# Kernel optimization log

Hardware: AMD Instinct MI355X
Metric: run time of the kernel (lower is better)

Reference implementation:

```python
import jax, jax.numpy as jnp
import numpy as np

EPS = 1e-5  # config.layer_norm_epsilon

def setup_inputs() -> dict:
    key = jax.random.key(0)
    ks = jax.random.split(key, 8)
    B, S, D, BOT, N = 8, 2048, 1024, 400, 25
    x = jax.random.normal(ks[0], (B, S, D), dtype=jnp.float32)
    alphas = jax.random.uniform(ks[1], (N,), dtype=jnp.float32) / N
    W_down_all = jax.random.normal(ks[2], (N, BOT, D), dtype=jnp.float32) * 0.02
    W_up_all = jax.random.normal(ks[3], (N, D, BOT), dtype=jnp.float32) * 0.02
    b_down_all = jax.random.normal(ks[4], (N, BOT), dtype=jnp.float32) * 0.02
    b_up_all = jax.random.normal(ks[5], (N, D), dtype=jnp.float32) * 0.02
    W_ln_all = 1.0 + jax.random.normal(ks[6], (N, D), dtype=jnp.float32) * 0.02
    b_ln_all = jax.random.normal(ks[7], (N, D), dtype=jnp.float32) * 0.02
    return {"x": x, "alphas": alphas, "W_down_all": W_down_all, "W_up_all": W_up_all,
            "b_down_all": b_down_all, "b_up_all": b_up_all,
            "W_ln_all": W_ln_all, "b_ln_all": b_ln_all}

def reference(x, alphas, W_down_all, W_up_all, b_down_all, b_up_all, W_ln_all, b_ln_all):
    # Superposition: alpha-weighted sum of all adapters' parameters
    # (original python loop over 25 adapters -> single einsum per tensor).
    W_down = jnp.einsum('n,nbd->bd', alphas, W_down_all)  # [BOT, D]
    W_up   = jnp.einsum('n,ndb->db', alphas, W_up_all)    # [D, BOT]
    W_ln   = jnp.einsum('n,nd->d',  alphas, W_ln_all)     # [D]
    b_ln   = jnp.einsum('n,nd->d',  alphas, b_ln_all)     # [D]
    # b_up / b_down are merged in the original too but passed with bias=None: unused.

    # FAdapter: F.layer_norm with normalized_shape = x.shape[1:], i.e. normalize
    # jointly over (seq, embd) per batch element; ln weight/bias broadcast over seq.
    mu = jnp.mean(x, axis=(1, 2), keepdims=True)
    var = jnp.mean(jnp.square(x - mu), axis=(1, 2), keepdims=True)
    x_ = (x - mu) * jax.lax.rsqrt(var + EPS) * W_ln + b_ln  # [B,S,D]

    h = jax.nn.relu(jnp.einsum('bsd,od->bso', x_, W_down))  # [B,S,BOT], no bias
    x_ = jnp.einsum('bso,do->bsd', h, W_up)                 # [B,S,D],   no bias
    return x + x_
```

## Files before the change

### kernel.cpp

```cpp
#include <hip/hip_runtime.h>
#include <stdint.h>

#define NB   8
#define SS   2048
#define DD   1024
#define BOT  400
#define BOTP 512
#define NAD  25
#define LN_EPS 1e-5f
#define NCH  128

typedef __attribute__((ext_vector_type(8))) short bf8_t;
typedef __attribute__((ext_vector_type(4))) float fx4;

__device__ __forceinline__ unsigned short f2bf(float f) {
  unsigned int u = __float_as_uint(f);
  u = (u + 0x7FFFu + ((u >> 16) & 1u)) >> 16;
  return (unsigned short)u;
}
__device__ __forceinline__ uint32_t cvtpk(float lo, float hi) {
  uint32_t r;
  asm("v_cvt_pk_bf16_f32 %0, %1, %2" : "=v"(r) : "v"(lo), "v"(hi));
  return r;
}

__device__ __forceinline__ void gload16(void* lds, const void* g) {
  __builtin_amdgcn_global_load_lds(
      (const __attribute__((address_space(1))) void*)(uintptr_t)g,
      (__attribute__((address_space(3))) void*)(uint32_t)(uintptr_t)lds,
      16, 0, 0);
}

__global__ __launch_bounds__(256) void mixstats_kernel(
    const float* __restrict__ alphas,
    const float* __restrict__ WdAll, const float* __restrict__ WuAll,
    const float* __restrict__ wlnAll, const float* __restrict__ blnAll,
    const float* __restrict__ x,
    unsigned short* __restrict__ Wd, unsigned short* __restrict__ Wu,
    float* __restrict__ wln, float* __restrict__ bln,
    float* __restrict__ partials)
{
  const int tid = threadIdx.x;
  const int bid = blockIdx.x;

  if (bid >= 920) {
    const int g = bid - 920;
    const int b = g >> 7, c = g & 127;
    const float4* xb = (const float4*)(x + (size_t)b * SS * DD) + (size_t)c * 4096;
    float4 v[16];
#pragma unroll
    for (int i = 0; i < 16; ++i) v[i] = xb[i * 256 + tid];
    __builtin_amdgcn_sched_barrier(0);
    float s = 0.f, q = 0.f;
#pragma unroll
    for (int i = 0; i < 16; ++i) {
      s += v[i].x + v[i].y + v[i].z + v[i].w;
      q += v[i].x * v[i].x + v[i].y * v[i].y + v[i].z * v[i].z + v[i].w * v[i].w;
    }
#pragma unroll
    for (int off = 32; off > 0; off >>= 1) { s += __shfl_down(s, off); q += __shfl_down(q, off); }
    __shared__ float red[8];
    const int wave = tid >> 6, lane = tid & 63;
    if (!lane) { red[wave] = s; red[wave + 4] = q; }
    __syncthreads();
    if (!tid) {
      partials[(b * NCH + c) * 2]     = red[0] + red[1] + red[2] + red[3];
      partials[(b * NCH + c) * 2 + 1] = red[4] + red[5] + red[6] + red[7];
    }
    return;
  }

  __shared__ float a[NAD];
  if (tid < NAD) a[tid] = alphas[tid];
  __syncthreads();

  if (bid < 800) {
    const int g = (bid < 400 ? bid : bid - 400) * 256 + tid;
    const float4* src = (const float4*)(bid < 400 ? WdAll : WuAll) + g;
    float4 vals[NAD];
#pragma unroll
    for (int n = 0; n < NAD; ++n) vals[n] = src[(size_t)n * 102400];
    __builtin_amdgcn_sched_barrier(0);
    float4 acc = {0.f, 0.f, 0.f, 0.f};
#pragma unroll
    for (int n = 0; n < NAD; ++n) {
      acc.x += a[n] * vals[n].x; acc.y += a[n] * vals[n].y;
      acc.z += a[n] * vals[n].z; acc.w += a[n] * vals[n].w;
    }
    uint2 pk = { cvtpk(acc.x, acc.y), cvtpk(acc.z, acc.w) };
    if (bid < 400) {
      *(uint2*)(Wd + (size_t)g * 4) = pk;
    } else {
      const int d = g / 100, bg = g - d * 100;
      *(uint2*)(Wu + (size_t)d * BOTP + bg * 4) = pk;
    }
  } else if (bid < 808) {
    const int i = (bid - 800) * 256 + tid;
    const float* src = (i < DD) ? wlnAll : blnAll;
    const int j = (i < DD) ? i : (i - DD);
    float v[NAD];
#pragma unroll
    for (int n = 0; n < NAD; ++n) v[n] = src[(size_t)n * DD + j];
    __builtin_amdgcn_sched_barrier(0);
    float s = 0.f;
#pragma unroll
    for (int n = 0; n < NAD; ++n) s += a[n] * v[n];
    if (i < DD) wln[j] = s; else bln[j] = s;
  } else if (bid < 864) {
    const int t = (bid - 808) * 256 + tid;
    int4 z = {0, 0, 0, 0};
    *(int4*)(Wd + 400 * 1024 + (size_t)t * 8) = z;
  } else {
    const int t = (bid - 864) * 256 + tid;
    const int row = t / 14, c8 = t - row * 14;
    int4 z = {0, 0, 0, 0};
    *(int4*)(Wu + (size_t)row * BOTP + 400 + c8 * 8) = z;
  }
}

__global__ __launch_bounds__(256) void norm_kernel(const float* __restrict__ x,
    const float* __restrict__ partials, const float* __restrict__ wln,
    const float* __restrict__ bln, unsigned short* __restrict__ xn)
{
  const int b = blockIdx.y;
  double sd = 0.0, qd = 0.0;
#pragma unroll 8
  for (int i = 0; i < NCH; ++i) {
    sd += partials[(b * NCH + i) * 2];
    qd += partials[(b * NCH + i) * 2 + 1];
  }
  const float mu  = (float)(sd * (1.0 / 2097152.0));
  const float var = (float)(qd * (1.0 / 2097152.0)) - mu * mu;
  const float rs  = rsqrtf(var + LN_EPS);

  const float4* xb = (const float4*)(x + (size_t)b * SS * DD);
  uint2* xnb = (uint2*)(xn + (size_t)b * SS * DD);
#pragma unroll
  for (int it = 0; it < 8; ++it) {
    const int idx = blockIdx.x * 2048 + it * 256 + threadIdx.x;
    const int dg = idx & 255;
    const float4 v = xb[idx];
    const float4 w = *(const float4*)&wln[dg * 4];
    const float4 bb = *(const float4*)&bln[dg * 4];
    const float s1x = rs * w.x, s1y = rs * w.y, s1z = rs * w.z, s1w = rs * w.w;
    uint2 pk;
    pk.x = cvtpk((v.x - mu) * s1x + bb.x, (v.y - mu) * s1y + bb.y);
    pk.y = cvtpk((v.z - mu) * s1z + bb.z, (v.w - mu) * s1w + bb.w);
    xnb[idx] = pk;
  }
}

template <int KDIM, int NBN, bool RELU>
__global__ __launch_bounds__(256) void gemm_bt(
    const unsigned short* __restrict__ A, const unsigned short* __restrict__ Bm,
    const float* __restrict__ Xres, float* __restrict__ Cf,
    unsigned short* __restrict__ Cb, int N)
{
  __shared__ char smraw[32768];
  unsigned short* As = (unsigned short*)smraw;
  unsigned short* Bs = (unsigned short*)(smraw + 16384);

  const int tid = threadIdx.x, wave = tid >> 6, lane = tid & 63;
  const int wr = wave >> 1, wc = wave & 1;
  const int cpx = gridDim.x >> 3;
  const int bid = (blockIdx.x & 7) * cpx + (blockIdx.x >> 3);
  const int bcol = bid & (NBN - 1), brow = bid / NBN;
  const unsigned short* Ab = A + (size_t)(brow * 128) * KDIM;
  const unsigned short* Bb = Bm + (size_t)(bcol * 128) * KDIM;

  auto stageM = [&](unsigned short* S, const unsigned short* P, int k0) {
#pragma unroll
    for (int i = 0; i < 4; ++i) {
      const int r = (i & 1) * 64 + wave * 16 + (lane >> 2);
      const int c = (i >> 1) * 32 + (lane & 3) * 8;
      gload16(&S[i * 2048 + wave * 512], P + (size_t)r * KDIM + k0 + c);
    }
  };

  fx4 acc[4][4] = {};
#pragma unroll 1
  for (int t = 0; t < KDIM / 64; ++t) {
    stageM(As, Ab, t * 64);
    stageM(Bs, Bb, t * 64);
    __syncthreads();
#pragma unroll
    for (int kk = 0; kk < 2; ++kk) {
      bf8_t af[4], bf[4];
      const int ko = kk * 4096 + (lane >> 4) * 8;
#pragma unroll
      for (int m = 0; m < 4; ++m)
        af[m] = *(const bf8_t*)&As[ko + (wr * 64 + m * 16 + (lane & 15)) * 32];
#pragma unroll
      for (int n = 0; n < 4; ++n)
        bf[n] = *(const bf8_t*)&Bs[ko + (wc * 64 + n * 16 + (lane & 15)) * 32];
#pragma unroll
      for (int m = 0; m < 4; ++m)
#pragma unroll
        for (int n = 0; n < 4; ++n)
          acc[m][n] = __builtin_amdgcn_mfma_f32_16x16x32_bf16(af[m], bf[n], acc[m][n], 0, 0, 0);
    }
    __syncthreads();
  }

  if constexpr (RELU) {
    unsigned short* Hs = (unsigned short*)smraw;
    const int r0l = wr * 64 + ((lane >> 4) << 2);
    const int c0l = wc * 64 + (lane & 15);
#pragma unroll
    for (int m = 0; m < 4; ++m)
#pragma unroll
      for (int n = 0; n < 4; ++n)
#pragma unroll
        for (int j = 0; j < 4; ++j) {
          float v = acc[m][n][j];
          Hs[(r0l + m * 16 + j) * 128 + (c0l + n * 16)] = f2bf(v > 0.f ? v : 0.f);
        }
    __syncthreads();
    const size_t outbase = (size_t)(brow * 128) * N + (size_t)bcol * 128;
#pragma unroll
    for (int i = 0; i < 8; ++i) {
      const int idx = i * 256 + tid;
      const int row = idx >> 4, colg = idx & 15;
      *(int4*)(Cb + outbase + (size_t)row * N + colg * 8) = *(const int4*)&Hs[row * 128 + colg * 8];
    }
  } else {
    float* Fs = (float*)smraw;
#pragma unroll
    for (int h2 = 0; h2 < 2; ++h2) {
      if (wr == h2) {
        const int c0l = wc * 64 + (lane & 15);
        const int rj = (lane >> 4) << 2;
#pragma unroll
        for (int m = 0; m < 4; ++m)
#pragma unroll
          for (int n = 0; n < 4; ++n)
#pragma unroll
            for (int j = 0; j < 4; ++j)
              Fs[(m * 16 + rj + j) * 128 + (c0l + n * 16)] = acc[m][n][j];
      }
      __syncthreads();
      const size_t gb = (size_t)(brow * 128 + h2 * 64) * N + (size_t)bcol * 128;
#pragma unroll
      for (int i = 0; i < 8; ++i) {
        const int idx = i * 256 + tid;
        const int row = idx >> 5, cg = idx & 31;
        const float4 f = *(const float4*)&Fs[row * 128 + cg * 4];
        const float4 xr = *(const float4*)&Xres[gb + (size_t)row * N + cg * 4];
        float4 o = { f.x + xr.x, f.y + xr.y, f.z + xr.z, f.w + xr.w };
        *(float4*)&Cf[gb + (size_t)row * N + cg * 4] = o;
      }
      __syncthreads();
    }
  }
}

extern "C" void kernel_launch(void* const* d_in, const int* in_sizes, int n_in,
                              void* d_out, int out_size, void* d_ws, size_t ws_size,
                              hipStream_t stream)
{
  const float* x      = (const float*)d_in[0];
  const float* alphas = (const float*)d_in[1];
  const float* WdAll  = (const float*)d_in[2];
  const float* WuAll  = (const float*)d_in[3];
  const float* wlnAll = (const float*)d_in[6];
  const float* blnAll = (const float*)d_in[7];
  float* out = (float*)d_out;

  char* ws = (char*)d_ws;
  unsigned short* Wd  = (unsigned short*)ws;
  unsigned short* Wu  = (unsigned short*)(ws + (1u << 20));
  float* wln          = (float*)(ws + (2u << 20));
  float* bln          = wln + DD;
  float* partials     = bln + DD;
  unsigned short* xn  = (unsigned short*)(ws + (3u << 20));
  unsigned short* h   = (unsigned short*)(ws + (35u << 20));

  mixstats_kernel<<<1944, 256, 0, stream>>>(alphas, WdAll, WuAll, wlnAll, blnAll, x,
                                            Wd, Wu, wln, bln, partials);
  norm_kernel<<<dim3(256, NB), 256, 0, stream>>>(x, partials, wln, bln, xn);
  gemm_bt<1024, 4, true ><<<512,  256, 0, stream>>>(xn, Wd, nullptr, nullptr, h, BOTP);
  gemm_bt<512,  8, false><<<1024, 256, 0, stream>>>(h, Wu, x, out, nullptr, DD);
}
```

Before: 265.2 us.

## Triple-buffer LDS tiles with async prefetch two K-steps ahead in GEMM

The bf16 MFMA GEMM moves from a single-buffered 64-wide K loop, with two barriers per step, to a three-stage ring of 32-wide K tiles. Each stage is prefetched two iterations ahead with direct-to-LDS loads, and a partial vmcnt wait plus one barrier per step lets global loads overlap the MFMA compute. This costs more LDS (48KB), which may reduce occupancy, and it doubles the number of loop iterations because each step covers half the K width.

```diff
diff --git a/kernel.cpp b/kernel.cpp
--- a/kernel.cpp
+++ b/kernel.cpp
@@ -156,9 +156,7 @@
     const float* __restrict__ Xres, float* __restrict__ Cf,
     unsigned short* __restrict__ Cb, int N)
 {
-  __shared__ char smraw[32768];
-  unsigned short* As = (unsigned short*)smraw;
-  unsigned short* Bs = (unsigned short*)(smraw + 16384);
+  __shared__ char smraw[49152];
 
   const int tid = threadIdx.x, wave = tid >> 6, lane = tid & 63;
   const int wr = wave >> 1, wc = wave & 1;
@@ -168,39 +166,63 @@
   const unsigned short* Ab = A + (size_t)(brow * 128) * KDIM;
   const unsigned short* Bb = Bm + (size_t)(bcol * 128) * KDIM;
 
-  auto stageM = [&](unsigned short* S, const unsigned short* P, int k0) {
-#pragma unroll
-    for (int i = 0; i < 4; ++i) {
-      const int r = (i & 1) * 64 + wave * 16 + (lane >> 2);
-      const int c = (i >> 1) * 32 + (lane & 3) * 8;
-      gload16(&S[i * 2048 + wave * 512], P + (size_t)r * KDIM + k0 + c);
+  auto stage = [&](int buf, int k0) {
+    unsigned short* S = (unsigned short*)(smraw + buf * 16384);
+#pragma unroll
+    for (int i = 0; i < 2; ++i) {
+      const int basee = (i * 256 + wave * 64) * 8;
+      const int e   = basee + lane * 8;
+      const int row = e >> 5, col = e & 31;
+      gload16(&S[basee],        Ab + (size_t)row * KDIM + k0 + col);
+      gload16(&S[4096 + basee], Bb + (size_t)row * KDIM + k0 + col);
     }
   };
 
   fx4 acc[4][4] = {};
+  auto compute = [&](int buf) {
+    const unsigned short* As = (const unsigned short*)(smraw + buf * 16384);
+    const unsigned short* Bs = As + 4096;
+    bf8_t af[4], bf[4];
+    const int hi8 = (lane >> 4) * 8;
+#pragma unroll
+    for (int m = 0; m < 4; ++m)
+      af[m] = *(const bf8_t*)&As[(wr * 64 + m * 16 + (lane & 15)) * 32 + hi8];
+#pragma unroll
+    for (int n = 0; n < 4; ++n)
+      bf[n] = *(const bf8_t*)&Bs[(wc * 64 + n * 16 + (lane & 15)) * 32 + hi8];
+#pragma unroll
+    for (int m = 0; m < 4; ++m)
+#pragma unroll
+      for (int n = 0; n < 4; ++n)
+        acc[m][n] = __builtin_amdgcn_mfma_f32_16x16x32_bf16(af[m], bf[n], acc[m][n], 0, 0, 0);
+  };
+
+  constexpr int NT = KDIM / 32;
+
+  stage(0, 0);
+  stage(1, 32);
+  asm volatile("s_waitcnt vmcnt(4)" ::: "memory");
+  __builtin_amdgcn_s_barrier();
+  __builtin_amdgcn_sched_barrier(0);
+
+  int r = 0, w = 2;
 #pragma unroll 1
-  for (int t = 0; t < KDIM / 64; ++t) {
-    stageM(As, Ab, t * 64);
-    stageM(Bs, Bb, t * 64);
-    __syncthreads();
-#pragma unroll
-    for (int kk = 0; kk < 2; ++kk) {
-      bf8_t af[4], bf[4];
-      const int ko = kk * 4096 + (lane >> 4) * 8;
-#pragma unroll
-      for (int m = 0; m < 4; ++m)
-        af[m] = *(const bf8_t*)&As[ko + (wr * 64 + m * 16 + (lane & 15)) * 32];
-#pragma unroll
-      for (int n = 0; n < 4; ++n)
-        bf[n] = *(const bf8_t*)&Bs[ko + (wc * 64 + n * 16 + (lane & 15)) * 32];
-#pragma unroll
-      for (int m = 0; m < 4; ++m)
-#pragma unroll
-        for (int n = 0; n < 4; ++n)
-          acc[m][n] = __builtin_amdgcn_mfma_f32_16x16x32_bf16(af[m], bf[n], acc[m][n], 0, 0, 0);
-    }
-    __syncthreads();
-  }
+  for (int t = 0; t < NT - 2; ++t) {
+    stage(w, (t + 2) * 32);
+    compute(r);
+    asm volatile("s_waitcnt vmcnt(4)" ::: "memory");
+    __builtin_amdgcn_s_barrier();
+    __builtin_amdgcn_sched_barrier(0);
+    r = (r == 2) ? 0 : r + 1;
+    w = (w == 2) ? 0 : w + 1;
+  }
+  compute(r);
+  asm volatile("s_waitcnt vmcnt(0)" ::: "memory");
+  __builtin_amdgcn_s_barrier();
+  __builtin_amdgcn_sched_barrier(0);
+  r = (r == 2) ? 0 : r + 1;
+  compute(r);
+  __syncthreads();
 
   if constexpr (RELU) {
     unsigned short* Hs = (unsigned short*)smraw;
```

After: 264.4 us. Within noise of the previous version (-0.3%).
